# Performance work log

Measured on AMD Instinct MI355X. Metric: run time of the kernel, lower is better.

## Reference

```python
import jax, jax.numpy as jnp
import numpy as np

RF = 16       # receptive_field
STRIDE = 16   # sim_strides
ALPHA = 0.3   # tf.keras LeakyReLU default alpha
EPS = 1e-3    # tf.keras BatchNormalization default epsilon


def _leaky(x):
    return jnp.where(x > 0, x, ALPHA * x)


def _bn_train(x, gamma, beta):
    # training-mode batch norm over (B, H, W), channel-last
    mu = jnp.mean(x, axis=(0, 1, 2))
    var = jnp.var(x, axis=(0, 1, 2))
    return (x - mu) * jax.lax.rsqrt(var + EPS) * gamma + beta


def _cbl(x, W, gamma, beta):
    # 1x1 conv (== channel matmul) + BN + LeakyReLU
    y = jnp.einsum('bhwc,cd->bhwd', x, W)
    return _leaky(_bn_train(y, gamma, beta))


def setup_inputs() -> dict:
    key = jax.random.key(0)
    ks = jax.random.split(key, 4)
    B, H, Wd, C = 4, 64, 64, 256
    s = 1.0 / np.sqrt(C)
    return {
        'inputs': jax.random.normal(ks[0], (B, H, Wd, C), jnp.float32),
        'Wq': jax.random.normal(ks[1], (C, C), jnp.float32) * s,
        'gq': jnp.ones((C,), jnp.float32), 'bq': jnp.zeros((C,), jnp.float32),
        'Wk': jax.random.normal(ks[2], (C, C), jnp.float32) * s,
        'gk': jnp.ones((C,), jnp.float32), 'bk': jnp.zeros((C,), jnp.float32),
        'Wv': jax.random.normal(ks[3], (C, C), jnp.float32) * s,
        'gv': jnp.ones((C,), jnp.float32), 'bv': jnp.zeros((C,), jnp.float32),
        'g1': jnp.ones((C,), jnp.float32), 'b1': jnp.zeros((C,), jnp.float32),
    }


def _windows(x):
    # x: [B,H,W,C] -> [B, nH*nW, RF, RF, C] overlapping-capable window gather
    H, Wd = x.shape[1], x.shape[2]
    nH = (H - RF) // STRIDE + 1
    nW = (Wd - RF) // STRIDE + 1
    ih = (jnp.arange(nH) * STRIDE)[:, None] + jnp.arange(RF)[None, :]  # [nH,RF]
    iw = (jnp.arange(nW) * STRIDE)[:, None] + jnp.arange(RF)[None, :]  # [nW,RF]
    xw = x[:, ih][:, :, :, iw]            # [B,nH,RF,nW,RF,C]
    xw = xw.transpose(0, 1, 3, 2, 4, 5)   # [B,nH,nW,RF,RF,C]
    return xw.reshape(x.shape[0], nH * nW, RF, RF, x.shape[3])


def reference(inputs, Wq, gq, bq, Wk, gk, bk, Wv, gv, bv, g1, b1):
    Q = _cbl(inputs, Wq, gq, bq)   # [B,H,W,C]
    K = _cbl(inputs, Wk, gk, bk)
    V = _cbl(inputs, Wv, gv, bv)
    C = Q.shape[-1]
    Kw = _windows(K)               # [B,N,RF,RF,C]
    Vw = _windows(V)
    # full-Q x window-K attention, summed over windows (matches nested loop)
    scores = jnp.einsum('bijc,bnpqc->bnijpq', Q, Kw) / jnp.sqrt(jnp.asarray(C, Q.dtype))
    scores = _leaky(scores)
    yout = jnp.einsum('bnijpq,bnpqc->bijc', scores, Vw)  # sum over windows n
    y = _bn_train(yout, g1, b1)
    # softmax jointly over spatial axes (1,2)
    m = jnp.max(y, axis=(1, 2), keepdims=True)
    e = jnp.exp(y - m)
    return e / jnp.sum(e, axis=(1, 2), keepdims=True)
```

## Files before the change

kernel.cpp:

```cpp
#include <hip/hip_runtime.h>
#include <stdint.h>


typedef __attribute__((ext_vector_type(8)))  short short8;
typedef __attribute__((ext_vector_type(4)))  float f32x4;
typedef __attribute__((ext_vector_type(16))) float f32x16;
typedef __attribute__((ext_vector_type(4)))  unsigned short ushort4v;

#define ALPHA 0.3f
#define EPS   1e-3
#define NTOT  16384.0

__device__ __forceinline__ unsigned short f2bf(float f){
  unsigned u = __float_as_uint(f);
  u += 0x7FFFu + ((u>>16)&1u);
  return (unsigned short)(u>>16);
}
__device__ __forceinline__ float lrelu(float x){ return x > 0.f ? x : ALPHA*x; }

__global__ __launch_bounds__(256)
void k_cvt(const float* __restrict__ X, unsigned short* __restrict__ Xb){
  int i = (blockIdx.x*256 + threadIdx.x)*4;
  float4 v = *(const float4*)(X + i);
  ushort4v o; o.x = f2bf(v.x); o.y = f2bf(v.y); o.z = f2bf(v.z); o.w = f2bf(v.w);
  *(ushort4v*)(Xb + i) = o;
}

__global__ __launch_bounds__(256)
void k_wtrans(const float* __restrict__ Wq,
              const float* __restrict__ Wk,
              const float* __restrict__ Wv,
              unsigned short* __restrict__ Wt){
  int o = blockIdx.x*256 + threadIdx.x;
  int p = o >> 16, rem = o & 65535;
  int j = rem >> 8, c = rem & 255;
  const float* W = (p==0) ? Wq : ((p==1) ? Wk : Wv);
  Wt[o] = f2bf(W[c*256 + j]);
}

__global__ __launch_bounds__(256)
void k_qkv_gemm(const unsigned short* __restrict__ X,
                const unsigned short* __restrict__ Wt,
                float* __restrict__ Y){
  __shared__ __align__(16) unsigned short At[64*264];
  __shared__ __align__(16) unsigned short Bt[64*264];
  int tid = threadIdx.x;
  int mb = blockIdx.x, nb = blockIdx.y;
#pragma unroll
  for (int it = 0; it < 8; ++it){
    int s = it*256 + tid;
    int row = s >> 5, ch = s & 31;
    uint4 a = *(const uint4*)(X  + ((size_t)(mb*64 + row))*256 + ch*8);
    uint4 b = *(const uint4*)(Wt + ((size_t)(nb*64 + row))*256 + ch*8);
    *(uint4*)(At + row*264 + ch*8) = a;
    *(uint4*)(Bt + row*264 + ch*8) = b;
  }
  __syncthreads();
  int lane = tid & 63, wv = tid >> 6;
  int ln15 = lane & 15, quad = lane >> 4;
  int rw = (wv & 1)*32, cw = (wv >> 1)*32;
  f32x4 acc[2][2] = {};
#pragma unroll
  for (int ks = 0; ks < 8; ++ks){
    short8 afr[2], bfr[2];
#pragma unroll
    for (int mt = 0; mt < 2; ++mt){
      int r = rw + mt*16 + ln15;
      afr[mt] = *(const short8*)(At + r*264 + (ks*4+quad)*8);
    }
#pragma unroll
    for (int nt = 0; nt < 2; ++nt){
      int r = cw + nt*16 + ln15;
      bfr[nt] = *(const short8*)(Bt + r*264 + (ks*4+quad)*8);
    }
#pragma unroll
    for (int mt = 0; mt < 2; ++mt)
#pragma unroll
      for (int nt = 0; nt < 2; ++nt)
        acc[mt][nt] = __builtin_amdgcn_mfma_f32_16x16x32_bf16(afr[mt], bfr[nt], acc[mt][nt], 0,0,0);
  }
#pragma unroll
  for (int mt = 0; mt < 2; ++mt)
#pragma unroll
    for (int nt = 0; nt < 2; ++nt)
#pragma unroll
      for (int r = 0; r < 4; ++r){
        int row = mb*64 + rw + mt*16 + quad*4 + r;
        int col = nb*64 + cw + nt*16 + ln15;
        Y[(size_t)row*768 + col] = acc[mt][nt][r];
      }
}

__global__ __launch_bounds__(256)
void k_stats1(const float* __restrict__ Y, double* __restrict__ st){
  int tid = threadIdx.x;
  int r0 = blockIdx.x * 32;
  float sum[3] = {0,0,0}, sq[3] = {0,0,0};
#pragma unroll 4
  for (int r = 0; r < 32; ++r){
    const float* row = Y + (size_t)(r0 + r)*768;
#pragma unroll
    for (int cg = 0; cg < 3; ++cg){
      float v = row[cg*256 + tid];
      sum[cg] += v; sq[cg] += v*v;
    }
  }
#pragma unroll
  for (int cg = 0; cg < 3; ++cg){
    atomicAdd(&st[cg*256 + tid], (double)sum[cg]);
    atomicAdd(&st[768 + cg*256 + tid], (double)sq[cg]);
  }
}

__global__ __launch_bounds__(256)
void k_coef(const double* __restrict__ st,
            const float* __restrict__ gq, const float* __restrict__ bq,
            const float* __restrict__ gk, const float* __restrict__ bk,
            const float* __restrict__ gv, const float* __restrict__ bv,
            float* __restrict__ scv, float* __restrict__ shv){
  int cc = blockIdx.x*256 + threadIdx.x;
  int proj = cc >> 8, c = cc & 255;
  double mu  = st[cc]     * (1.0/NTOT);
  double var = st[768+cc] * (1.0/NTOT) - mu*mu;
  double g = (proj==0) ? gq[c] : (proj==1) ? gk[c] : gv[c];
  double b = (proj==0) ? bq[c] : (proj==1) ? bk[c] : bv[c];
  double sc = g / sqrt(var + EPS);
  scv[cc] = (float)sc;
  shv[cc] = (float)(b - mu*sc);
}

__global__ __launch_bounds__(256)
void k_bn_qk(const float* __restrict__ Y,
             const float* __restrict__ scv, const float* __restrict__ shv,
             unsigned short* __restrict__ Qf, unsigned short* __restrict__ Kf){
  int idx = blockIdx.x*256 + threadIdx.x;
  int t = idx >> 6, cb = idx & 63;
  int proj = cb >> 5, cbl = cb & 31;
  int ch0 = cbl*8;
  const float* src = Y + (size_t)t*768 + proj*256 + ch0;
  float4 v0 = *(const float4*)(src);
  float4 v1 = *(const float4*)(src + 4);
  const float* sc = scv + proj*256 + ch0;
  const float* sh = shv + proj*256 + ch0;
  unsigned short r[8];
  r[0]=f2bf(lrelu(v0.x*sc[0]+sh[0])); r[1]=f2bf(lrelu(v0.y*sc[1]+sh[1]));
  r[2]=f2bf(lrelu(v0.z*sc[2]+sh[2])); r[3]=f2bf(lrelu(v0.w*sc[3]+sh[3]));
  r[4]=f2bf(lrelu(v1.x*sc[4]+sh[4])); r[5]=f2bf(lrelu(v1.y*sc[5]+sh[5]));
  r[6]=f2bf(lrelu(v1.z*sc[6]+sh[6])); r[7]=f2bf(lrelu(v1.w*sc[7]+sh[7]));
  uint4 u;
  u.x = (unsigned)r[0] | ((unsigned)r[1]<<16);
  u.y = (unsigned)r[2] | ((unsigned)r[3]<<16);
  u.z = (unsigned)r[4] | ((unsigned)r[5]<<16);
  u.w = (unsigned)r[6] | ((unsigned)r[7]<<16);
  int g = t >> 5, l31r = t & 31;
  int ks = cbl >> 1, l5c = cbl & 1;
  unsigned short* dst = (proj ? Kf : Qf) + ((size_t)((g*16 + ks)*64 + l5c*32 + l31r))*8;
  *(uint4*)dst = u;
}

__global__ __launch_bounds__(256)
void k_bn_v(const float* __restrict__ Y,
            const float* __restrict__ scv, const float* __restrict__ shv,
            unsigned short* __restrict__ Vf){
  __shared__ unsigned short tile[64][66];
  int tid = threadIdx.x;
  int pt = blockIdx.x, ct = blockIdx.y, b = blockIdx.z;
  int cl = tid & 63, rq = tid >> 6;
  int c  = ct*64 + cl;
  float sc = scv[512 + c], sh = shv[512 + c];
#pragma unroll 4
  for (int k = 0; k < 16; ++k){
    int r = k*4 + rq;
    size_t t = (size_t)b*4096 + pt*64 + r;
    float v = Y[t*768 + 512 + c];
    tile[r][cl] = f2bf(lrelu(v*sc + sh));
  }
  __syncthreads();
#pragma unroll
  for (int it = 0; it < 2; ++it){
    int m = it*256 + tid;
    int c2 = m >> 3, kg = m & 7;
    int ch = ct*64 + c2;
    int gc = b*8 + (ch >> 5), l31c = ch & 31;
    int kp = pt*4 + (kg >> 1), l5k = kg & 1;
    unsigned short r0 = tile[kg*8+0][c2], r1 = tile[kg*8+1][c2];
    unsigned short r2 = tile[kg*8+2][c2], r3 = tile[kg*8+3][c2];
    unsigned short r4 = tile[kg*8+4][c2], r5 = tile[kg*8+5][c2];
    unsigned short r6 = tile[kg*8+6][c2], r7 = tile[kg*8+7][c2];
    uint4 u;
    u.x = (unsigned)r0 | ((unsigned)r1<<16);
    u.y = (unsigned)r2 | ((unsigned)r3<<16);
    u.z = (unsigned)r4 | ((unsigned)r5<<16);
    u.w = (unsigned)r6 | ((unsigned)r7<<16);
    *(uint4*)(Vf + ((size_t)((gc*256 + kp)*64 + l5k*32 + l31c))*8) = u;
  }
}

__global__ __launch_bounds__(512, 4)
void k_attn(const unsigned short* __restrict__ Qf,
            const unsigned short* __restrict__ Kf,
            const unsigned short* __restrict__ Vf,
            float* __restrict__ P0, float* __restrict__ P1){
  __shared__ __align__(16) unsigned short Ql[64*256];
  __shared__ __align__(16) unsigned short Sl[64*264];
  int tid = threadIdx.x;
  int blk = blockIdx.x;
  int qt = blk >> 3, combo = blk & 7;
  int b = combo >> 1, half = combo & 1;
  int q0 = qt*64;
  int lane = tid & 63, w = tid >> 6;
  int l31 = lane & 31, l5 = lane >> 5;
  float* P = half ? P1 : P0;

  int gq0 = b*128 + qt*2;
  {
    const uint4* src = (const uint4*)(Qf + (size_t)gq0*8192);
    uint4* dst = (uint4*)Ql;
#pragma unroll
    for (int it = 0; it < 4; ++it) dst[it*512 + tid] = src[it*512 + tid];
  }
  __syncthreads();

  f32x16 acc2[2] = {};
  int gk0 = b*128 + half*64 + w;
  const unsigned short* kb = Kf + (size_t)gk0*8192 + lane*8;
  const unsigned short* vb = Vf + ((size_t)((b*8 + w)*256 + half*128))*512 + lane*8;
  const unsigned short* qa0 = Ql + lane*8;
  const unsigned short* qa1 = Ql + 16*512 + lane*8;

  for (int kt = 0; kt < 8; ++kt){
    f32x16 a1[2] = {};
    const unsigned short* kbt = kb + (size_t)kt*8*8192;
#pragma unroll
    for (int ks = 0; ks < 16; ++ks){
      short8 kf = *(const short8*)(kbt + ks*512);
      short8 q0v = *(const short8*)(qa0 + ks*512);
      short8 q1v = *(const short8*)(qa1 + ks*512);
      a1[0] = __builtin_amdgcn_mfma_f32_32x32x16_bf16(q0v, kf, a1[0], 0, 0, 0);
      a1[1] = __builtin_amdgcn_mfma_f32_32x32x16_bf16(q1v, kf, a1[1], 0, 0, 0);
    }
    __syncthreads();
#pragma unroll
    for (int reg = 0; reg < 16; ++reg){
      int rloc = (reg & 3) + 8*(reg >> 2) + 4*l5;
      Sl[rloc*264 + w*32 + l31]        = f2bf(lrelu(a1[0][reg]*0.0625f));
      Sl[(32 + rloc)*264 + w*32 + l31] = f2bf(lrelu(a1[1][reg]*0.0625f));
    }
    __syncthreads();
    const unsigned short* vbt = vb + (size_t)kt*16*512;
#pragma unroll
    for (int kk = 0; kk < 16; ++kk){
      short8 vf = *(const short8*)(vbt + kk*512);
      short8 s0 = *(const short8*)(Sl + (     l31)*264 + kk*16 + l5*8);
      short8 s1 = *(const short8*)(Sl + (32 + l31)*264 + kk*16 + l5*8);
      acc2[0] = __builtin_amdgcn_mfma_f32_32x32x16_bf16(s0, vf, acc2[0], 0, 0, 0);
      acc2[1] = __builtin_amdgcn_mfma_f32_32x32x16_bf16(s1, vf, acc2[1], 0, 0, 0);
    }
  }
#pragma unroll
  for (int c = 0; c < 2; ++c)
#pragma unroll
    for (int reg = 0; reg < 16; ++reg){
      int row = q0 + c*32 + (reg & 3) + 8*(reg >> 2) + 4*l5;
      P[((size_t)b*4096 + row)*256 + w*32 + l31] = acc2[c][reg];
    }
}

__global__ __launch_bounds__(256)
void k_red(const float* __restrict__ P0, const float* __restrict__ P1,
           float* __restrict__ yout, double* __restrict__ st){
  int tid = threadIdx.x;
  int r0 = blockIdx.x*32;
  double sum = 0, sq = 0;
#pragma unroll 4
  for (int r = 0; r < 32; ++r){
    size_t idx = (size_t)(r0 + r)*256 + tid;
    float v = P0[idx] + P1[idx];
    yout[idx] = v;
    sum += v; sq += (double)v*v;
  }
  atomicAdd(&st[1536 + tid], sum);
  atomicAdd(&st[1792 + tid], sq);
}

__global__ __launch_bounds__(256)
void k_soft1(const float* __restrict__ yout, const double* __restrict__ st,
             const float* __restrict__ g1, float* __restrict__ sums){
  __shared__ float red[256];
  __shared__ float sA[64], sK[64];
  int tid = threadIdx.x;
  int chunk = blockIdx.x, ct = blockIdx.y, b = blockIdx.z;
  int cl = tid & 63, pg = tid >> 6;
  int c = ct*64 + cl;
  if (tid < 64){
    int cc = ct*64 + tid;
    double mu  = st[1536 + cc]*(1.0/NTOT);
    double var = st[1792 + cc]*(1.0/NTOT) - mu*mu;
    double a = g1[cc] / sqrt(var + EPS);
    sA[tid] = (float)a;
    sK[tid] = (float)(a*mu);
  }
  __syncthreads();
  float a = sA[cl], K = sK[cl];
  float s = 0.f;
  const float* base = yout + ((size_t)b*4096 + chunk*256)*256 + c;
#pragma unroll 4
  for (int k = 0; k < 64; ++k){
    float v = base[(size_t)(pg + k*4)*256];
    s += __expf(v*a - K);
  }
  red[tid] = s;
  __syncthreads();
  if (tid < 64){
    float tot = red[tid] + red[64+tid] + red[128+tid] + red[192+tid];
    atomicAdd(&sums[b*256 + ct*64 + tid], tot);
  }
}

__global__ __launch_bounds__(256)
void k_soft2(const float* __restrict__ yout, const double* __restrict__ st,
             const float* __restrict__ g1, const float* __restrict__ sums,
             float* __restrict__ out){
  __shared__ float sA[64], sK[64], sR[64];
  int tid = threadIdx.x;
  int chunk = blockIdx.x, ct = blockIdx.y, b = blockIdx.z;
  int cl = tid & 63, pg = tid >> 6;
  int c = ct*64 + cl;
  if (tid < 64){
    int cc = ct*64 + tid;
    double mu  = st[1536 + cc]*(1.0/NTOT);
    double var = st[1792 + cc]*(1.0/NTOT) - mu*mu;
    double a = g1[cc] / sqrt(var + EPS);
    sA[tid] = (float)a;
    sK[tid] = (float)(a*mu);
    sR[tid] = 1.f / sums[b*256 + cc];
  }
  __syncthreads();
  float a = sA[cl], K = sK[cl], rl = sR[cl];
  const float* base = yout + ((size_t)b*4096 + chunk*256)*256 + c;
  float* obase = out + ((size_t)b*4096 + chunk*256)*256 + c;
#pragma unroll 4
  for (int k = 0; k < 64; ++k){
    size_t idx = (size_t)(pg + k*4)*256;
    obase[idx] = __expf(base[idx]*a - K) * rl;
  }
}

extern "C" void kernel_launch(void* const* d_in, const int* in_sizes, int n_in,
                              void* d_out, int out_size, void* d_ws, size_t ws_size,
                              hipStream_t stream){
  (void)in_sizes; (void)n_in; (void)out_size; (void)ws_size;
  const float* X  = (const float*)d_in[0];
  const float* Wq = (const float*)d_in[1];
  const float* gq = (const float*)d_in[2];
  const float* bq = (const float*)d_in[3];
  const float* Wk = (const float*)d_in[4];
  const float* gk = (const float*)d_in[5];
  const float* bk = (const float*)d_in[6];
  const float* Wv = (const float*)d_in[7];
  const float* gv = (const float*)d_in[8];
  const float* bv = (const float*)d_in[9];
  const float* g1 = (const float*)d_in[10];

  char* ws = (char*)d_ws;
  double*         st   = (double*)ws;
  float*          sums = (float*)(ws + 16384);
  float*          scv  = (float*)(ws + 20480);
  float*          shv  = (float*)(ws + 23552);
  unsigned short* Wt   = (unsigned short*)(ws + 26624);
  unsigned short* Xb   = (unsigned short*)(ws + 419840);
  float*          Y    = (float*)(ws + 8808448);
  unsigned short* Kf   = (unsigned short*)(ws + 59140096);
  unsigned short* Vf   = (unsigned short*)(ws + 67528704);
  unsigned short* Qf   = Xb;
  float*          P0   = Y;
  float*          P1   = (float*)((char*)Y + 16777216);
  float*          yo   = (float*)((char*)Y + 33554432);

  hipMemsetAsync(st, 0, 20480, stream);
  k_cvt     <<<4096, 256, 0, stream>>>(X, Xb);
  k_wtrans  <<<768, 256, 0, stream>>>(Wq, Wk, Wv, Wt);
  k_qkv_gemm<<<dim3(256,12), 256, 0, stream>>>(Xb, Wt, Y);
  k_stats1  <<<512, 256, 0, stream>>>(Y, st);
  k_coef    <<<3, 256, 0, stream>>>(st, gq, bq, gk, bk, gv, bv, scv, shv);
  k_bn_qk   <<<4096, 256, 0, stream>>>(Y, scv, shv, Qf, Kf);
  k_bn_v    <<<dim3(64,4,4), 256, 0, stream>>>(Y, scv, shv, Vf);
  k_attn    <<<512, 512, 0, stream>>>(Qf, Kf, Vf, P0, P1);
  k_red     <<<512, 256, 0, stream>>>(P0, P1, yo, st);
  k_soft1   <<<dim3(16,4,4), 256, 0, stream>>>(yo, st, g1, sums);
  k_soft2   <<<dim3(16,4,4), 256, 0, stream>>>(yo, st, g1, sums, (float*)d_out);
}
```

Baseline: 252.8 us.

## Fuse input conversion and BN stats into QKV GEMM, retile attention warps

The fp32-to-bf16 input conversion moves into the QKV GEMM prologue. The GEMM now loops over all 12 column blocks per row tile, reading weights from a pre-swizzled MFMA fragment layout in global memory. Per-channel sum and sum-of-squares are accumulated in the GEMM epilogue with float atomics, which removes the separate stats kernel and the conversion kernel. The attention kernel is re-partitioned so each warp computes two key/value column groups for one query half, with vectorized score stores and padded LDS. Float atomics for the BN statistics trade some accuracy against the old double accumulation, and the GEMM now has only 256 blocks.

```diff
diff --git a/kernel.cpp b/kernel.cpp
--- a/kernel.cpp
+++ b/kernel.cpp
@@ -19,109 +19,100 @@
 __device__ __forceinline__ float lrelu(float x){ return x > 0.f ? x : ALPHA*x; }
 
 __global__ __launch_bounds__(256)
-void k_cvt(const float* __restrict__ X, unsigned short* __restrict__ Xb){
-  int i = (blockIdx.x*256 + threadIdx.x)*4;
-  float4 v = *(const float4*)(X + i);
-  ushort4v o; o.x = f2bf(v.x); o.y = f2bf(v.y); o.z = f2bf(v.z); o.w = f2bf(v.w);
-  *(ushort4v*)(Xb + i) = o;
-}
-
-__global__ __launch_bounds__(256)
 void k_wtrans(const float* __restrict__ Wq,
               const float* __restrict__ Wk,
               const float* __restrict__ Wv,
-              unsigned short* __restrict__ Wt){
-  int o = blockIdx.x*256 + threadIdx.x;
-  int p = o >> 16, rem = o & 65535;
-  int j = rem >> 8, c = rem & 255;
-  const float* W = (p==0) ? Wq : ((p==1) ? Wk : Wv);
-  Wt[o] = f2bf(W[c*256 + j]);
-}
-
-__global__ __launch_bounds__(256)
-void k_qkv_gemm(const unsigned short* __restrict__ X,
-                const unsigned short* __restrict__ Wt,
-                float* __restrict__ Y){
+              unsigned short* __restrict__ Wtf){
+  int t = blockIdx.x*256 + threadIdx.x;
+  int cg = t >> 9, r = t & 511;
+  int ks = r >> 6, lane = r & 63;
+  int col = cg*16 + (lane & 15);
+  int proj = col >> 8, d = col & 255;
+  const float* W = (proj==0) ? Wq : ((proj==1) ? Wk : Wv);
+  int c0 = ks*32 + (lane >> 4)*8;
+  unsigned short o[8];
+#pragma unroll
+  for (int j = 0; j < 8; ++j) o[j] = f2bf(W[(size_t)(c0+j)*256 + d]);
+  uint4 u;
+  u.x = (unsigned)o[0] | ((unsigned)o[1]<<16);
+  u.y = (unsigned)o[2] | ((unsigned)o[3]<<16);
+  u.z = (unsigned)o[4] | ((unsigned)o[5]<<16);
+  u.w = (unsigned)o[6] | ((unsigned)o[7]<<16);
+  *(uint4*)(Wtf + (size_t)t*8) = u;
+}
+
+__global__ __launch_bounds__(256)
+void k_qkv_gemm(const float* __restrict__ X,
+                const unsigned short* __restrict__ Wtf,
+                float* __restrict__ Y, float* __restrict__ stf){
   __shared__ __align__(16) unsigned short At[64*264];
-  __shared__ __align__(16) unsigned short Bt[64*264];
-  int tid = threadIdx.x;
-  int mb = blockIdx.x, nb = blockIdx.y;
-#pragma unroll
-  for (int it = 0; it < 8; ++it){
+  int tid = threadIdx.x;
+  int mb = blockIdx.x;
+#pragma unroll
+  for (int it = 0; it < 16; ++it){
     int s = it*256 + tid;
-    int row = s >> 5, ch = s & 31;
-    uint4 a = *(const uint4*)(X  + ((size_t)(mb*64 + row))*256 + ch*8);
-    uint4 b = *(const uint4*)(Wt + ((size_t)(nb*64 + row))*256 + ch*8);
-    *(uint4*)(At + row*264 + ch*8) = a;
-    *(uint4*)(Bt + row*264 + ch*8) = b;
+    int row = s >> 6, c4 = s & 63;
+    float4 v = *(const float4*)(X + ((size_t)(mb*64+row))*256 + c4*4);
+    ushort4v o; o.x=f2bf(v.x); o.y=f2bf(v.y); o.z=f2bf(v.z); o.w=f2bf(v.w);
+    *(ushort4v*)(At + row*264 + c4*4) = o;
   }
   __syncthreads();
   int lane = tid & 63, wv = tid >> 6;
   int ln15 = lane & 15, quad = lane >> 4;
   int rw = (wv & 1)*32, cw = (wv >> 1)*32;
-  f32x4 acc[2][2] = {};
-#pragma unroll
-  for (int ks = 0; ks < 8; ++ks){
-    short8 afr[2], bfr[2];
-#pragma unroll
-    for (int mt = 0; mt < 2; ++mt){
-      int r = rw + mt*16 + ln15;
-      afr[mt] = *(const short8*)(At + r*264 + (ks*4+quad)*8);
+  for (int nb = 0; nb < 12; ++nb){
+    f32x4 acc[2][2] = {};
+#pragma unroll
+    for (int ks = 0; ks < 8; ++ks){
+      short8 afr[2], bfr[2];
+#pragma unroll
+      for (int mt = 0; mt < 2; ++mt)
+        afr[mt] = *(const short8*)(At + (rw + mt*16 + ln15)*264 + (ks*4+quad)*8);
+#pragma unroll
+      for (int nt = 0; nt < 2; ++nt){
+        int cg = nb*4 + (wv>>1)*2 + nt;
+        bfr[nt] = *(const short8*)(Wtf + ((size_t)(cg*8 + ks))*512 + lane*8);
+      }
+#pragma unroll
+      for (int mt = 0; mt < 2; ++mt)
+#pragma unroll
+        for (int nt = 0; nt < 2; ++nt)
+          acc[mt][nt] = __builtin_amdgcn_mfma_f32_16x16x32_bf16(afr[mt], bfr[nt], acc[mt][nt], 0,0,0);
     }
 #pragma unroll
     for (int nt = 0; nt < 2; ++nt){
-      int r = cw + nt*16 + ln15;
-      bfr[nt] = *(const short8*)(Bt + r*264 + (ks*4+quad)*8);
-    }
-#pragma unroll
-    for (int mt = 0; mt < 2; ++mt)
-#pragma unroll
-      for (int nt = 0; nt < 2; ++nt)
-        acc[mt][nt] = __builtin_amdgcn_mfma_f32_16x16x32_bf16(afr[mt], bfr[nt], acc[mt][nt], 0,0,0);
-  }
-#pragma unroll
-  for (int mt = 0; mt < 2; ++mt)
-#pragma unroll
-    for (int nt = 0; nt < 2; ++nt)
-#pragma unroll
-      for (int r = 0; r < 4; ++r){
-        int row = mb*64 + rw + mt*16 + quad*4 + r;
-        int col = nb*64 + cw + nt*16 + ln15;
-        Y[(size_t)row*768 + col] = acc[mt][nt][r];
+      float s = 0.f, q = 0.f;
+#pragma unroll
+      for (int mt = 0; mt < 2; ++mt)
+#pragma unroll
+        for (int r = 0; r < 4; ++r){
+          int row = mb*64 + rw + mt*16 + quad*4 + r;
+          int col = nb*64 + cw + nt*16 + ln15;
+          float v = acc[mt][nt][r];
+          Y[(size_t)row*768 + col] = v;
+          s += v; q += v*v;
+        }
+      s += __shfl_xor(s, 16); s += __shfl_xor(s, 32);
+      q += __shfl_xor(q, 16); q += __shfl_xor(q, 32);
+      if (lane < 16){
+        int col = nb*64 + cw + nt*16 + lane;
+        atomicAdd(&stf[col], s);
+        atomicAdd(&stf[768 + col], q);
       }
-}
-
-__global__ __launch_bounds__(256)
-void k_stats1(const float* __restrict__ Y, double* __restrict__ st){
-  int tid = threadIdx.x;
-  int r0 = blockIdx.x * 32;
-  float sum[3] = {0,0,0}, sq[3] = {0,0,0};
-#pragma unroll 4
-  for (int r = 0; r < 32; ++r){
-    const float* row = Y + (size_t)(r0 + r)*768;
-#pragma unroll
-    for (int cg = 0; cg < 3; ++cg){
-      float v = row[cg*256 + tid];
-      sum[cg] += v; sq[cg] += v*v;
-    }
-  }
-#pragma unroll
-  for (int cg = 0; cg < 3; ++cg){
-    atomicAdd(&st[cg*256 + tid], (double)sum[cg]);
-    atomicAdd(&st[768 + cg*256 + tid], (double)sq[cg]);
-  }
-}
-
-__global__ __launch_bounds__(256)
-void k_coef(const double* __restrict__ st,
+    }
+  }
+}
+
+__global__ __launch_bounds__(256)
+void k_coef(const float* __restrict__ stf,
             const float* __restrict__ gq, const float* __restrict__ bq,
             const float* __restrict__ gk, const float* __restrict__ bk,
             const float* __restrict__ gv, const float* __restrict__ bv,
             float* __restrict__ scv, float* __restrict__ shv){
   int cc = blockIdx.x*256 + threadIdx.x;
   int proj = cc >> 8, c = cc & 255;
-  double mu  = st[cc]     * (1.0/NTOT);
-  double var = st[768+cc] * (1.0/NTOT) - mu*mu;
+  double mu  = (double)stf[cc]     * (1.0/NTOT);
+  double var = (double)stf[768+cc] * (1.0/NTOT) - mu*mu;
   double g = (proj==0) ? gq[c] : (proj==1) ? gk[c] : gv[c];
   double b = (proj==0) ? bq[c] : (proj==1) ? bk[c] : bv[c];
   double sc = g / sqrt(var + EPS);
@@ -202,7 +193,7 @@
             const unsigned short* __restrict__ Vf,
             float* __restrict__ P0, float* __restrict__ P1){
   __shared__ __align__(16) unsigned short Ql[64*256];
-  __shared__ __align__(16) unsigned short Sl[64*264];
+  __shared__ __align__(16) unsigned short Sl[64*268];
   int tid = threadIdx.x;
   int blk = blockIdx.x;
   int qt = blk >> 3, combo = blk & 7;
@@ -210,11 +201,11 @@
   int q0 = qt*64;
   int lane = tid & 63, w = tid >> 6;
   int l31 = lane & 31, l5 = lane >> 5;
+  int qh = w & 1, grp = w >> 1;
   float* P = half ? P1 : P0;
 
-  int gq0 = b*128 + qt*2;
   {
-    const uint4* src = (const uint4*)(Qf + (size_t)gq0*8192);
+    const uint4* src = (const uint4*)(Qf + (size_t)(b*128 + qt*2)*8192);
     uint4* dst = (uint4*)Ql;
 #pragma unroll
     for (int it = 0; it < 4; ++it) dst[it*512 + tid] = src[it*512 + tid];
@@ -222,53 +213,62 @@
   __syncthreads();
 
   f32x16 acc2[2] = {};
-  int gk0 = b*128 + half*64 + w;
-  const unsigned short* kb = Kf + (size_t)gk0*8192 + lane*8;
-  const unsigned short* vb = Vf + ((size_t)((b*8 + w)*256 + half*128))*512 + lane*8;
-  const unsigned short* qa0 = Ql + lane*8;
-  const unsigned short* qa1 = Ql + 16*512 + lane*8;
+  const unsigned short* kb  = Kf + (size_t)(b*128 + half*64 + grp*2)*8192 + lane*8;
+  const unsigned short* vb0 = Vf + ((size_t)((b*8 + grp*2    )*256 + half*128))*512 + lane*8;
+  const unsigned short* vb1 = Vf + ((size_t)((b*8 + grp*2 + 1)*256 + half*128))*512 + lane*8;
+  const unsigned short* qa  = Ql + (size_t)(qh*16)*512 + lane*8;
+  unsigned short* swr = Sl + (qh*32 + l31)*268 + grp*64 + l5*4;
 
   for (int kt = 0; kt < 8; ++kt){
     f32x16 a1[2] = {};
     const unsigned short* kbt = kb + (size_t)kt*8*8192;
 #pragma unroll
     for (int ks = 0; ks < 16; ++ks){
-      short8 kf = *(const short8*)(kbt + ks*512);
-      short8 q0v = *(const short8*)(qa0 + ks*512);
-      short8 q1v = *(const short8*)(qa1 + ks*512);
-      a1[0] = __builtin_amdgcn_mfma_f32_32x32x16_bf16(q0v, kf, a1[0], 0, 0, 0);
-      a1[1] = __builtin_amdgcn_mfma_f32_32x32x16_bf16(q1v, kf, a1[1], 0, 0, 0);
+      short8 qv = *(const short8*)(qa + ks*512);
+      short8 k0 = *(const short8*)(kbt + ks*512);
+      short8 k1 = *(const short8*)(kbt + 8192 + ks*512);
+      a1[0] = __builtin_amdgcn_mfma_f32_32x32x16_bf16(k0, qv, a1[0], 0, 0, 0);
+      a1[1] = __builtin_amdgcn_mfma_f32_32x32x16_bf16(k1, qv, a1[1], 0, 0, 0);
     }
     __syncthreads();
 #pragma unroll
+    for (int kc = 0; kc < 2; ++kc)
+#pragma unroll
+      for (int rg = 0; rg < 4; ++rg){
+        unsigned short p0 = f2bf(lrelu(a1[kc][rg*4+0]*0.0625f));
+        unsigned short p1 = f2bf(lrelu(a1[kc][rg*4+1]*0.0625f));
+        unsigned short p2 = f2bf(lrelu(a1[kc][rg*4+2]*0.0625f));
+        unsigned short p3 = f2bf(lrelu(a1[kc][rg*4+3]*0.0625f));
+        uint2 u;
+        u.x = (unsigned)p0 | ((unsigned)p1<<16);
+        u.y = (unsigned)p2 | ((unsigned)p3<<16);
+        *(uint2*)(swr + kc*32 + rg*8) = u;
+      }
+    __syncthreads();
+    const unsigned short* v0t = vb0 + (size_t)kt*8192;
+    const unsigned short* v1t = vb1 + (size_t)kt*8192;
+#pragma unroll
+    for (int kk = 0; kk < 16; ++kk){
+      short8 sf = *(const short8*)(Sl + (qh*32 + l31)*268 + kk*16 + l5*8);
+      short8 v0 = *(const short8*)(v0t + kk*512);
+      short8 v1 = *(const short8*)(v1t + kk*512);
+      acc2[0] = __builtin_amdgcn_mfma_f32_32x32x16_bf16(sf, v0, acc2[0], 0, 0, 0);
+      acc2[1] = __builtin_amdgcn_mfma_f32_32x32x16_bf16(sf, v1, acc2[1], 0, 0, 0);
+    }
+  }
+#pragma unroll
+  for (int ct = 0; ct < 2; ++ct)
+#pragma unroll
     for (int reg = 0; reg < 16; ++reg){
-      int rloc = (reg & 3) + 8*(reg >> 2) + 4*l5;
-      Sl[rloc*264 + w*32 + l31]        = f2bf(lrelu(a1[0][reg]*0.0625f));
-      Sl[(32 + rloc)*264 + w*32 + l31] = f2bf(lrelu(a1[1][reg]*0.0625f));
-    }
-    __syncthreads();
-    const unsigned short* vbt = vb + (size_t)kt*16*512;
-#pragma unroll
-    for (int kk = 0; kk < 16; ++kk){
-      short8 vf = *(const short8*)(vbt + kk*512);
-      short8 s0 = *(const short8*)(Sl + (     l31)*264 + kk*16 + l5*8);
-      short8 s1 = *(const short8*)(Sl + (32 + l31)*264 + kk*16 + l5*8);
-      acc2[0] = __builtin_amdgcn_mfma_f32_32x32x16_bf16(s0, vf, acc2[0], 0, 0, 0);
-      acc2[1] = __builtin_amdgcn_mfma_f32_32x32x16_bf16(s1, vf, acc2[1], 0, 0, 0);
-    }
-  }
-#pragma unroll
-  for (int c = 0; c < 2; ++c)
-#pragma unroll
-    for (int reg = 0; reg < 16; ++reg){
-      int row = q0 + c*32 + (reg & 3) + 8*(reg >> 2) + 4*l5;
-      P[((size_t)b*4096 + row)*256 + w*32 + l31] = acc2[c][reg];
+      int row = q0 + qh*32 + (reg & 3) + 8*(reg >> 2) + 4*l5;
+      int col = grp*64 + ct*32 + l31;
+      P[((size_t)b*4096 + row)*256 + col] = acc2[ct][reg];
     }
 }
 
 __global__ __launch_bounds__(256)
 void k_red(const float* __restrict__ P0, const float* __restrict__ P1,
-           float* __restrict__ yout, double* __restrict__ st){
+           float* __restrict__ yout, double* __restrict__ std_){
   int tid = threadIdx.x;
   int r0 = blockIdx.x*32;
   double sum = 0, sq = 0;
@@ -279,12 +279,12 @@
     yout[idx] = v;
     sum += v; sq += (double)v*v;
   }
-  atomicAdd(&st[1536 + tid], sum);
-  atomicAdd(&st[1792 + tid], sq);
-}
-
-__global__ __launch_bounds__(256)
-void k_soft1(const float* __restrict__ yout, const double* __restrict__ st,
+  atomicAdd(&std_[tid], sum);
+  atomicAdd(&std_[256 + tid], sq);
+}
+
+__global__ __launch_bounds__(256)
+void k_soft1(const float* __restrict__ yout, const double* __restrict__ std_,
              const float* __restrict__ g1, float* __restrict__ sums){
   __shared__ float red[256];
   __shared__ float sA[64], sK[64];
@@ -294,8 +294,8 @@
   int c = ct*64 + cl;
   if (tid < 64){
     int cc = ct*64 + tid;
-    double mu  = st[1536 + cc]*(1.0/NTOT);
-    double var = st[1792 + cc]*(1.0/NTOT) - mu*mu;
+    double mu  = std_[cc]*(1.0/NTOT);
+    double var = std_[256 + cc]*(1.0/NTOT) - mu*mu;
     double a = g1[cc] / sqrt(var + EPS);
     sA[tid] = (float)a;
     sK[tid] = (float)(a*mu);
@@ -318,7 +318,7 @@
 }
 
 __global__ __launch_bounds__(256)
-void k_soft2(const float* __restrict__ yout, const double* __restrict__ st,
+void k_soft2(const float* __restrict__ yout, const double* __restrict__ std_,
              const float* __restrict__ g1, const float* __restrict__ sums,
              float* __restrict__ out){
   __shared__ float sA[64], sK[64], sR[64];
@@ -328,8 +328,8 @@
   int c = ct*64 + cl;
   if (tid < 64){
     int cc = ct*64 + tid;
-    double mu  = st[1536 + cc]*(1.0/NTOT);
-    double var = st[1792 + cc]*(1.0/NTOT) - mu*mu;
+    double mu  = std_[cc]*(1.0/NTOT);
+    double var = std_[256 + cc]*(1.0/NTOT) - mu*mu;
     double a = g1[cc] / sqrt(var + EPS);
     sA[tid] = (float)a;
     sK[tid] = (float)(a*mu);
@@ -363,30 +363,28 @@
   const float* g1 = (const float*)d_in[10];
 
   char* ws = (char*)d_ws;
-  double*         st   = (double*)ws;
-  float*          sums = (float*)(ws + 16384);
-  float*          scv  = (float*)(ws + 20480);
-  float*          shv  = (float*)(ws + 23552);
-  unsigned short* Wt   = (unsigned short*)(ws + 26624);
-  unsigned short* Xb   = (unsigned short*)(ws + 419840);
-  float*          Y    = (float*)(ws + 8808448);
-  unsigned short* Kf   = (unsigned short*)(ws + 59140096);
-  unsigned short* Vf   = (unsigned short*)(ws + 67528704);
-  unsigned short* Qf   = Xb;
+  float*          stf  = (float*)ws;
+  double*         std_ = (double*)(ws + 6144);
+  float*          sums = (float*)(ws + 10240);
+  float*          scv  = (float*)(ws + 14336);
+  float*          shv  = (float*)(ws + 17408);
+  unsigned short* Wtf  = (unsigned short*)(ws + 20480);
+  float*          Y    = (float*)(ws + 413696);
+  unsigned short* Qf   = (unsigned short*)(ws + 50745344);
+  unsigned short* Kf   = (unsigned short*)(ws + 59133952);
+  unsigned short* Vf   = (unsigned short*)(ws + 67522560);
   float*          P0   = Y;
   float*          P1   = (float*)((char*)Y + 16777216);
   float*          yo   = (float*)((char*)Y + 33554432);
 
-  hipMemsetAsync(st, 0, 20480, stream);
-  k_cvt     <<<4096, 256, 0, stream>>>(X, Xb);
-  k_wtrans  <<<768, 256, 0, stream>>>(Wq, Wk, Wv, Wt);
-  k_qkv_gemm<<<dim3(256,12), 256, 0, stream>>>(Xb, Wt, Y);
-  k_stats1  <<<512, 256, 0, stream>>>(Y, st);
-  k_coef    <<<3, 256, 0, stream>>>(st, gq, bq, gk, bk, gv, bv, scv, shv);
+  hipMemsetAsync(ws, 0, 14336, stream);
+  k_wtrans  <<<96, 256, 0, stream>>>(Wq, Wk, Wv, Wtf);
+  k_qkv_gemm<<<256, 256, 0, stream>>>(X, Wtf, Y, stf);
+  k_coef    <<<3, 256, 0, stream>>>(stf, gq, bq, gk, bk, gv, bv, scv, shv);
   k_bn_qk   <<<4096, 256, 0, stream>>>(Y, scv, shv, Qf, Kf);
   k_bn_v    <<<dim3(64,4,4), 256, 0, stream>>>(Y, scv, shv, Vf);
   k_attn    <<<512, 512, 0, stream>>>(Qf, Kf, Vf, P0, P1);
-  k_red     <<<512, 256, 0, stream>>>(P0, P1, yo, st);
-  k_soft1   <<<dim3(16,4,4), 256, 0, stream>>>(yo, st, g1, sums);
-  k_soft2   <<<dim3(16,4,4), 256, 0, stream>>>(yo, st, g1, sums, (float*)d_out);
-}
+  k_red     <<<512, 256, 0, stream>>>(P0, P1, yo, std_);
+  k_soft1   <<<dim3(16,4,4), 256, 0, stream>>>(yo, std_, g1, sums);
+  k_soft2   <<<dim3(16,4,4), 256, 0, stream>>>(yo, std_, g1, sums, (float*)d_out);
+}
```

After: 281.3 us. 1.11x slower.
